# Performance work log

Hardware: AMD Instinct MI355X
Metric: run time of the kernel (lower is better)

The kernel has to match this reference:

```python
import jax, jax.numpy as jnp
from jax import lax
import numpy as np

TAU = 2.0      # LIF membrane time constant
VTH = 1.0      # spikingjelly LIFNode default v_threshold
ALPHA = 2.0    # spikingjelly surrogate.ATan default alpha

# Heaviside spike with ATan surrogate gradient (spikingjelly semantics)
@jax.custom_vjp
def spike(x):
    return (x >= 0.0).astype(x.dtype)

def _spike_fwd(x):
    return spike(x), x

def _spike_bwd(x, g):
    sg = (ALPHA / 2.0) / (1.0 + (jnp.pi / 2.0 * ALPHA * x) ** 2)
    return (g * sg,)

spike.defvjp(_spike_fwd, _spike_bwd)

def lif_step(v, x):
    # decay_input=True, v_reset=0.0, hard reset (spikingjelly LIFNode defaults)
    v = v + (x - v) / TAU
    s = spike(v - VTH)
    v = v * (1.0 - s)
    return v, s

def conv1d_same(x, k):
    # x: [N, L], k: [K]  -> depthwise-style 1D conv with SAME padding
    y = lax.conv_general_dilated(x[:, None, :], k[None, None, :], (1,), 'SAME')
    return y[:, 0, :]

def setup_inputs() -> dict:
    key = jax.random.key(0)
    ks = jax.random.split(key, 16)
    N, T, D, C, NC = 4096, 16, 700, 128, 20
    def lin(kw, kb, fout, fin):
        s = 1.0 / np.sqrt(fin)
        W = jax.random.uniform(kw, (fout, fin), jnp.float32, -s, s)
        b = jax.random.uniform(kb, (fout,), jnp.float32, -s, s)
        return W, b
    x = jax.random.normal(ks[0], (N, T, D), jnp.float32)
    W_in, b_in = lin(ks[1], ks[2], C, D)
    W_rec, b_rec = lin(ks[3], ks[4], C, C)
    W2, b2 = lin(ks[5], ks[6], C, C)
    k_t = jax.random.normal(ks[7], (3,), jnp.float32) * 0.5   # TATCA temporal conv, kernel_size_t=3
    k_c = jax.random.normal(ks[8], (3,), jnp.float32) * 0.5   # TATCA channel conv
    W_p, b_p = lin(ks[9], ks[10], C, C)
    W_out, b_out = lin(ks[11], ks[12], NC, C)
    return {"x": x, "W_in": W_in, "b_in": b_in, "W_rec": W_rec, "b_rec": b_rec,
            "W2": W2, "b2": b2, "k_t": k_t, "k_c": k_c,
            "W_p": W_p, "b_p": b_p, "W_out": W_out, "b_out": b_out}

def reference(x, W_in, b_in, W_rec, b_rec, W2, b2, k_t, k_c, W_p, b_p, W_out, b_out):
    N, T, D = x.shape
    C = W_in.shape[0]
    z = jnp.zeros((N, C), x.dtype)

    def step(carry, frame):
        v1, v2, spikes_last = carry
        inp = frame @ W_in.T + b_in + spikes_last @ W_rec.T + b_rec
        v1, s1 = lif_step(v1, inp)
        x2 = s1 @ W2.T + b2
        v2, feat = lif_step(v2, x2)
        return (v1, v2, s1), feat

    xs = jnp.transpose(x, (1, 0, 2))          # [T, N, D]
    _, features = lax.scan(step, (z, z, z), xs)  # [T, N, C]

    # TATCA_1D: temporal attention (conv over T, kernel 3) x channel attention (conv over C)
    t_att = jax.nn.sigmoid(conv1d_same(features.mean(2).T, k_t)).T   # [T, N]
    c_att = jax.nn.sigmoid(conv1d_same(features.mean(0), k_c))       # [N, C]
    attended = features * t_att[:, :, None] * c_att[None, :, :]

    def step2(v3, feat):
        h = feat @ W_p.T + b_p
        v3, s = lif_step(v3, h)
        return v3, s @ W_out.T + b_out

    _, outs = lax.scan(step2, z, attended)    # [T, N, num_classes]
    return outs.mean(0), features, attended
```

## Files before the change

kernel.cpp:

```cpp
#include <hip/hip_runtime.h>
#include <hip/hip_bf16.h>
#include <stdint.h>


typedef __attribute__((ext_vector_type(8))) _Float16 half8;
typedef __attribute__((ext_vector_type(4))) float f32x4;
typedef unsigned long long u64;

#define MFMA16F(a, b, c) __builtin_amdgcn_mfma_f32_16x16x32_f16(a, b, c, 0, 0, 0)

__device__ inline void gload16(const void* g, void* l) {
  __builtin_amdgcn_global_load_lds(
      (const __attribute__((address_space(1))) uint32_t*)g,
      (__attribute__((address_space(3))) uint32_t*)l, 16, 0, 0);
}

__device__ inline void splitf16(float4 q0, float4 q1, half8& hh, half8& ll) {
  float f[8] = {q0.x, q0.y, q0.z, q0.w, q1.x, q1.y, q1.z, q1.w};
  _Float16 H[8], L[8];
#pragma unroll
  for (int j = 0; j < 8; ++j) {
    _Float16 h1 = (_Float16)(f[j] * 16.0f);
    float r = fmaf((float)h1, -0.0625f, f[j]);
    L[j] = (_Float16)(r * 32768.0f);
    H[j] = h1;
  }
  __builtin_memcpy(&hh, H, 16);
  __builtin_memcpy(&ll, L, 16);
}

__global__ void k_prep(const float* __restrict__ Wr, const float* __restrict__ W2,
                       const float* __restrict__ Wp, const float* __restrict__ Win,
                       float* __restrict__ WrT, float* __restrict__ W2T,
                       float* __restrict__ WpT, ushort* __restrict__ F2) {
  int idx = blockIdx.x * blockDim.x + threadIdx.x;
  if (idx < 3 * 16384) {
    int sel = idx >> 14;
    int r = idx & 16383;
    int j = r >> 7, c = r & 127;
    const float* src = (sel == 0) ? Wr : (sel == 1) ? W2 : Wp;
    float* dst = (sel == 0) ? WrT : (sel == 1) ? W2T : WpT;
    dst[r] = src[c * 128 + j];
  } else {
    int i2 = idx - 49152;
    if (i2 >= 128 * 704) return;
    int c = i2 / 704, d = i2 - c * 704;
    float w = (d < 700) ? Win[c * 700 + d] : 0.f;
    _Float16 b1 = (_Float16)(w * 256.0f);
    float r = fmaf((float)b1, -0.00390625f, w);
    _Float16 b2 = (_Float16)(r * 524288.0f);
    ushort u1, u2;
    __builtin_memcpy(&u1, &b1, 2);
    __builtin_memcpy(&u2, &b2, 2);
    F2[i2] = u1;
    F2[90112 + i2] = u2;
  }
}

__global__ __launch_bounds__(512, 4) void k_gemm_mfma(
    const float* __restrict__ x, const ushort* __restrict__ F2,
    const float* __restrict__ b_in, const float* __restrict__ b_rec,
    float* __restrict__ XW) {
  __shared__ __align__(16) char lds[65536];

  const int tid = threadIdx.x;
  const int w = tid >> 6;
  const int l = tid & 63;
  const int blk = blockIdx.x;
  const int wr = w >> 2;
  const int wc = w & 3;

  const int jA = (((l & 7) ^ (l >> 3)) * 4);
  const int t_blk = (blk * 128) >> 12;
  const int n0_blk = (blk * 128) & 4095;
  int arow[2];
#pragma unroll
  for (int i = 0; i < 2; ++i) {
    int m = (w * 2 + i) * 8 + (l >> 3);
    arow[i] = ((n0_blk + m) * 16 + t_blk) * 700;
  }
  const ushort* bsrc[2];
  int bdst[2];
#pragma unroll
  for (int i = 0; i < 2; ++i) {
    int idx = w * 2 + i;
    int plane = idx >> 3, cg = idx & 7;
    int col = cg * 16 + (l >> 2);
    bsrc[i] = F2 + plane * 90112 + col * 704 + (((l & 3) ^ ((l >> 3) & 3)) * 8);
    bdst[i] = 16384 + plane * 8192 + cg * 1024;
  }
  const int adst = (w * 2) * 1024;

  const int lm = l & 15, kh = l >> 4;
  const int p0 = ((2 * kh) ^ (lm & 7)) * 16;
  const int p1 = ((2 * kh + 1) ^ (lm & 7)) * 16;
  const int bswz = (kh ^ ((lm >> 1) & 3)) * 16;
  int aoff[4], boff[2];
#pragma unroll
  for (int mf = 0; mf < 4; ++mf) aoff[mf] = (wr * 64 + mf * 16 + lm) * 128;
#pragma unroll
  for (int nf = 0; nf < 2; ++nf) boff[nf] = 16384 + (wc * 32 + nf * 16 + lm) * 64 + bswz;

  f32x4 acc_h[4][2], acc_m[4][2];
#pragma unroll
  for (int i = 0; i < 4; ++i)
#pragma unroll
    for (int j = 0; j < 2; ++j) {
      acc_h[i][j] = (f32x4){0.f, 0.f, 0.f, 0.f};
      acc_m[i][j] = (f32x4){0.f, 0.f, 0.f, 0.f};
    }

  auto STAGE = [&](int buf, int kt) {
    const int k0 = kt * 32;
    char* base = lds + buf * 32768;
#pragma unroll
    for (int i = 0; i < 2; ++i) {
      int k = k0 + jA;
      int off = (k < 700) ? (arow[i] + k) : 0;
      gload16(x + off, base + adst + i * 1024);
    }
#pragma unroll
    for (int i = 0; i < 2; ++i)
      gload16(bsrc[i] + k0, base + bdst[i]);
  };

  STAGE(0, 0);
  __syncthreads();
  int buf = 0;
  for (int kt = 0; kt < 22; ++kt) {
    if (kt + 1 < 22) STAGE(buf ^ 1, kt + 1);
    const char* base = lds + buf * 32768;
    half8 b1[2], b2[2];
#pragma unroll
    for (int nf = 0; nf < 2; ++nf) {
      const char* bb = base + boff[nf];
      b1[nf] = *(const half8*)(bb);
      b2[nf] = *(const half8*)(bb + 8192);
    }
#pragma unroll
    for (int mf = 0; mf < 4; ++mf) {
      const char* ab = base + aoff[mf];
      float4 q0 = *(const float4*)(ab + p0);
      float4 q1 = *(const float4*)(ab + p1);
      half8 a1, a2;
      splitf16(q0, q1, a1, a2);
#pragma unroll
      for (int nf = 0; nf < 2; ++nf) {
        acc_h[mf][nf] = MFMA16F(a1, b1[nf], acc_h[mf][nf]);
        acc_m[mf][nf] = MFMA16F(a1, b2[nf], acc_m[mf][nf]);
        acc_m[mf][nf] = MFMA16F(a2, b1[nf], acc_m[mf][nf]);
      }
    }
    __syncthreads();
    buf ^= 1;
  }

  const int outbase = blk * 128;
#pragma unroll
  for (int nf = 0; nf < 2; ++nf) {
    int col = wc * 32 + nf * 16 + lm;
    float bias = b_in[col] + b_rec[col];
#pragma unroll
    for (int mf = 0; mf < 4; ++mf) {
      int mrow = outbase + wr * 64 + mf * 16 + kh * 4;
#pragma unroll
      for (int r = 0; r < 4; ++r)
        XW[(size_t)(mrow + r) * 128 + col] =
            acc_h[mf][nf][r] * 0.000244140625f +
            acc_m[mf][nf][r] * 1.1920928955078125e-7f + bias;
    }
  }
}

__global__ __launch_bounds__(256) void k_scan(
    const float* __restrict__ XW, const float* __restrict__ WrT,
    const float* __restrict__ W2T, const float* __restrict__ b2,
    const float* __restrict__ WpT, const float* __restrict__ b_p,
    const float* __restrict__ W_out, const float* __restrict__ b_out,
    const float* __restrict__ k_t, const float* __restrict__ k_c,
    float* __restrict__ features, float* __restrict__ attended,
    float* __restrict__ out0) {
  const int tid = threadIdx.x;
  const int r = tid >> 7;
  const int c = tid & 127;
  const int n = blockIdx.x * 2 + r;
  const int wv = c >> 6;
  const int lane = tid & 63;

  __shared__ u64 smask[2][2];
  __shared__ u64 fmask[2][16][2];
  __shared__ float m0p[2][130];
  __shared__ float ta[2][16];
  __shared__ float ca[2][128];
  __shared__ float g[2][128];

  if (tid < 4) ((u64*)smask)[tid] = 0ull;
  float v1 = 0.f, v2 = 0.f, fsum = 0.f;
  const float b2c = b2[c];
  __syncthreads();

  for (int t = 0; t < 16; ++t) {
    float inp = XW[(size_t)((t << 12) | n) * 128 + c];
    u64 p0 = smask[r][0], p1 = smask[r][1];
    while (p0) { int j = __builtin_ctzll(p0); p0 &= p0 - 1; inp += WrT[j * 128 + c]; }
    while (p1) { int j = __builtin_ctzll(p1); p1 &= p1 - 1; inp += WrT[(64 + j) * 128 + c]; }
    v1 = v1 + (inp - v1) * 0.5f;
    bool s1 = (v1 - 1.0f) >= 0.f;
    v1 = s1 ? 0.f : v1;
    __syncthreads();
    u64 bm = __ballot((int)s1);
    if (lane == 0) smask[r][wv] = bm;
    __syncthreads();
    float x2 = b2c;
    u64 q0 = smask[r][0], q1 = smask[r][1];
    while (q0) { int j = __builtin_ctzll(q0); q0 &= q0 - 1; x2 += W2T[j * 128 + c]; }
    while (q1) { int j = __builtin_ctzll(q1); q1 &= q1 - 1; x2 += W2T[(64 + j) * 128 + c]; }
    v2 = v2 + (x2 - v2) * 0.5f;
    bool f = (v2 - 1.0f) >= 0.f;
    v2 = f ? 0.f : v2;
    float ff = f ? 1.f : 0.f;
    features[(size_t)((t << 12) | n) * 128 + c] = ff;
    fsum += ff;
    u64 fb = __ballot((int)f);
    if (lane == 0) fmask[r][t][wv] = fb;
  }

  m0p[r][c + 1] = fsum * (1.f / 16.f);
  if (c == 0) { m0p[r][0] = 0.f; m0p[r][129] = 0.f; }
  __syncthreads();

  if (c < 16) {
    float acc = 0.f;
#pragma unroll
    for (int j = 0; j < 3; ++j) {
      int tt = c - 1 + j;
      if (tt >= 0 && tt < 16) {
        float m = (float)(__popcll(fmask[r][tt][0]) + __popcll(fmask[r][tt][1])) * (1.f / 128.f);
        acc += k_t[j] * m;
      }
    }
    ta[r][c] = 1.f / (1.f + expf(-acc));
  }
  {
    float acc = k_c[0] * m0p[r][c] + k_c[1] * m0p[r][c + 1] + k_c[2] * m0p[r][c + 2];
    ca[r][c] = 1.f / (1.f + expf(-acc));
  }
  __syncthreads();

  float v3 = 0.f, ssum = 0.f;
  const float bpc = b_p[c];
  const float cac = ca[r][c];
  for (int t = 0; t < 16; ++t) {
    u64 m0 = fmask[r][t][0], m1 = fmask[r][t][1];
    float tat = ta[r][t];
    bool bit = ((wv ? m1 : m0) >> (c & 63)) & 1;
    float att = bit ? tat * cac : 0.f;
    attended[(size_t)((t << 12) | n) * 128 + c] = att;
    float h = bpc;
    while (m0) { int j = __builtin_ctzll(m0); m0 &= m0 - 1; h += (tat * ca[r][j]) * WpT[j * 128 + c]; }
    while (m1) { int j = __builtin_ctzll(m1); m1 &= m1 - 1; h += (tat * ca[r][64 + j]) * WpT[(64 + j) * 128 + c]; }
    v3 = v3 + (h - v3) * 0.5f;
    bool s = (v3 - 1.0f) >= 0.f;
    v3 = s ? 0.f : v3;
    ssum += s ? 1.f : 0.f;
  }
  g[r][c] = ssum * (1.f / 16.f);
  __syncthreads();
  if (c < 20) {
    float acc = b_out[c];
    for (int j = 0; j < 128; ++j) acc += g[r][j] * W_out[c * 128 + j];
    out0[n * 20 + c] = acc;
  }
}

extern "C" void kernel_launch(void* const* d_in, const int* in_sizes, int n_in,
                              void* d_out, int out_size, void* d_ws, size_t ws_size,
                              hipStream_t stream) {
  const float* x     = (const float*)d_in[0];
  const float* W_in  = (const float*)d_in[1];
  const float* b_in  = (const float*)d_in[2];
  const float* W_rec = (const float*)d_in[3];
  const float* b_rec = (const float*)d_in[4];
  const float* W2    = (const float*)d_in[5];
  const float* b2    = (const float*)d_in[6];
  const float* k_t   = (const float*)d_in[7];
  const float* k_c   = (const float*)d_in[8];
  const float* W_p   = (const float*)d_in[9];
  const float* b_p   = (const float*)d_in[10];
  const float* W_out = (const float*)d_in[11];
  const float* b_out = (const float*)d_in[12];

  float* out      = (float*)d_out;
  float* out0     = out;
  float* features = out + 81920;
  float* attended = out + 81920 + 8388608;
  float* XW       = attended;

  float* ws  = (float*)d_ws;
  float* WrT = ws;
  float* W2T = ws + 16384;
  float* WpT = ws + 32768;
  ushort* F2 = (ushort*)(ws + 49152);

  hipLaunchKernelGGL(k_prep, dim3(544), dim3(256), 0, stream,
                     W_rec, W2, W_p, W_in, WrT, W2T, WpT, F2);
  hipLaunchKernelGGL(k_gemm_mfma, dim3(512), dim3(512), 0, stream,
                     x, F2, b_in, b_rec, XW);
  hipLaunchKernelGGL(k_scan, dim3(2048), dim3(256), 0, stream,
                     XW, WrT, W2T, b2, WpT, b_p, W_out, b_out, k_t, k_c,
                     features, attended, out0);
}
```

Baseline: 92.99 us.

## Fuse input GEMM with LIF scan via LDS-resident XW tiles

Merges the MFMA input-projection GEMM and the recurrent scan into one kernel. Each block now computes 128 rows as 8 samples × 16 timesteps, so every sample's full time series stays in the block, and the projection is staged in LDS instead of round-tripping through global memory. This removes the XW write and read and one launch. In exchange the scan runs with only 512 blocks of 4 samples per chunk in two serial chunks, which cuts parallelism for the latency-bound scan and adds block-wide barriers.

```diff
diff --git a/kernel.cpp b/kernel.cpp
--- a/kernel.cpp
+++ b/kernel.cpp
@@ -57,10 +57,15 @@
   }
 }
 
-__global__ __launch_bounds__(512, 4) void k_gemm_mfma(
+__global__ __launch_bounds__(512, 4) void k_gemm_scan(
     const float* __restrict__ x, const ushort* __restrict__ F2,
     const float* __restrict__ b_in, const float* __restrict__ b_rec,
-    float* __restrict__ XW) {
+    const float* __restrict__ WrT, const float* __restrict__ W2T,
+    const float* __restrict__ b2, const float* __restrict__ WpT,
+    const float* __restrict__ b_p, const float* __restrict__ W_out,
+    const float* __restrict__ b_out, const float* __restrict__ k_t,
+    const float* __restrict__ k_c, float* __restrict__ features,
+    float* __restrict__ attended, float* __restrict__ out0) {
   __shared__ __align__(16) char lds[65536];
 
   const int tid = threadIdx.x;
@@ -71,14 +76,10 @@
   const int wc = w & 3;
 
   const int jA = (((l & 7) ^ (l >> 3)) * 4);
-  const int t_blk = (blk * 128) >> 12;
-  const int n0_blk = (blk * 128) & 4095;
   int arow[2];
 #pragma unroll
-  for (int i = 0; i < 2; ++i) {
-    int m = (w * 2 + i) * 8 + (l >> 3);
-    arow[i] = ((n0_blk + m) * 16 + t_blk) * 700;
-  }
+  for (int i = 0; i < 2; ++i)
+    arow[i] = (blk * 128 + (w * 2 + i) * 8 + (l >> 3)) * 700;
   const ushort* bsrc[2];
   int bdst[2];
 #pragma unroll
@@ -130,12 +131,12 @@
   for (int kt = 0; kt < 22; ++kt) {
     if (kt + 1 < 22) STAGE(buf ^ 1, kt + 1);
     const char* base = lds + buf * 32768;
-    half8 b1[2], b2[2];
+    half8 b1[2], b2f[2];
 #pragma unroll
     for (int nf = 0; nf < 2; ++nf) {
       const char* bb = base + boff[nf];
       b1[nf] = *(const half8*)(bb);
-      b2[nf] = *(const half8*)(bb + 8192);
+      b2f[nf] = *(const half8*)(bb + 8192);
     }
 #pragma unroll
     for (int mf = 0; mf < 4; ++mf) {
@@ -147,7 +148,7 @@
 #pragma unroll
       for (int nf = 0; nf < 2; ++nf) {
         acc_h[mf][nf] = MFMA16F(a1, b1[nf], acc_h[mf][nf]);
-        acc_m[mf][nf] = MFMA16F(a1, b2[nf], acc_m[mf][nf]);
+        acc_m[mf][nf] = MFMA16F(a1, b2f[nf], acc_m[mf][nf]);
         acc_m[mf][nf] = MFMA16F(a2, b1[nf], acc_m[mf][nf]);
       }
     }
@@ -155,121 +156,124 @@
     buf ^= 1;
   }
 
-  const int outbase = blk * 128;
+  float bias[2];
 #pragma unroll
   for (int nf = 0; nf < 2; ++nf) {
     int col = wc * 32 + nf * 16 + lm;
-    float bias = b_in[col] + b_rec[col];
-#pragma unroll
-    for (int mf = 0; mf < 4; ++mf) {
-      int mrow = outbase + wr * 64 + mf * 16 + kh * 4;
-#pragma unroll
-      for (int r = 0; r < 4; ++r)
-        XW[(size_t)(mrow + r) * 128 + col] =
-            acc_h[mf][nf][r] * 0.000244140625f +
-            acc_m[mf][nf][r] * 1.1920928955078125e-7f + bias;
-    }
-  }
-}
-
-__global__ __launch_bounds__(256) void k_scan(
-    const float* __restrict__ XW, const float* __restrict__ WrT,
-    const float* __restrict__ W2T, const float* __restrict__ b2,
-    const float* __restrict__ WpT, const float* __restrict__ b_p,
-    const float* __restrict__ W_out, const float* __restrict__ b_out,
-    const float* __restrict__ k_t, const float* __restrict__ k_c,
-    float* __restrict__ features, float* __restrict__ attended,
-    float* __restrict__ out0) {
-  const int tid = threadIdx.x;
-  const int r = tid >> 7;
+    bias[nf] = b_in[col] + b_rec[col];
+  }
+
+  float* XWs = (float*)lds;
+  u64* smaskp = (u64*)(lds + 33792);
+  u64* fmaskp = (u64*)(lds + 33856);
+  float* tap = (float*)(lds + 34880);
+  float* m0p = (float*)(lds + 35136);
+  float* cap = (float*)(lds + 37216);
+  float* gp = (float*)(lds + 39264);
+
+  const int s = tid >> 7;
   const int c = tid & 127;
-  const int n = blockIdx.x * 2 + r;
-  const int wv = c >> 6;
+  const int wv = (tid >> 6) & 1;
   const int lane = tid & 63;
-
-  __shared__ u64 smask[2][2];
-  __shared__ u64 fmask[2][16][2];
-  __shared__ float m0p[2][130];
-  __shared__ float ta[2][16];
-  __shared__ float ca[2][128];
-  __shared__ float g[2][128];
-
-  if (tid < 4) ((u64*)smask)[tid] = 0ull;
-  float v1 = 0.f, v2 = 0.f, fsum = 0.f;
   const float b2c = b2[c];
-  __syncthreads();
-
-  for (int t = 0; t < 16; ++t) {
-    float inp = XW[(size_t)((t << 12) | n) * 128 + c];
-    u64 p0 = smask[r][0], p1 = smask[r][1];
-    while (p0) { int j = __builtin_ctzll(p0); p0 &= p0 - 1; inp += WrT[j * 128 + c]; }
-    while (p1) { int j = __builtin_ctzll(p1); p1 &= p1 - 1; inp += WrT[(64 + j) * 128 + c]; }
-    v1 = v1 + (inp - v1) * 0.5f;
-    bool s1 = (v1 - 1.0f) >= 0.f;
-    v1 = s1 ? 0.f : v1;
-    __syncthreads();
-    u64 bm = __ballot((int)s1);
-    if (lane == 0) smask[r][wv] = bm;
-    __syncthreads();
-    float x2 = b2c;
-    u64 q0 = smask[r][0], q1 = smask[r][1];
-    while (q0) { int j = __builtin_ctzll(q0); q0 &= q0 - 1; x2 += W2T[j * 128 + c]; }
-    while (q1) { int j = __builtin_ctzll(q1); q1 &= q1 - 1; x2 += W2T[(64 + j) * 128 + c]; }
-    v2 = v2 + (x2 - v2) * 0.5f;
-    bool f = (v2 - 1.0f) >= 0.f;
-    v2 = f ? 0.f : v2;
-    float ff = f ? 1.f : 0.f;
-    features[(size_t)((t << 12) | n) * 128 + c] = ff;
-    fsum += ff;
-    u64 fb = __ballot((int)f);
-    if (lane == 0) fmask[r][t][wv] = fb;
-  }
-
-  m0p[r][c + 1] = fsum * (1.f / 16.f);
-  if (c == 0) { m0p[r][0] = 0.f; m0p[r][129] = 0.f; }
-  __syncthreads();
-
-  if (c < 16) {
-    float acc = 0.f;
-#pragma unroll
-    for (int j = 0; j < 3; ++j) {
-      int tt = c - 1 + j;
-      if (tt >= 0 && tt < 16) {
-        float m = (float)(__popcll(fmask[r][tt][0]) + __popcll(fmask[r][tt][1])) * (1.f / 128.f);
-        acc += k_t[j] * m;
+  const float bpc = b_p[c];
+
+  for (int chunk = 0; chunk < 2; ++chunk) {
+    __syncthreads();
+    if (tid < 8) smaskp[tid] = 0ull;
+    if (wr == chunk) {
+#pragma unroll
+      for (int nf = 0; nf < 2; ++nf) {
+        int col = wc * 32 + nf * 16 + lm;
+#pragma unroll
+        for (int mf = 0; mf < 4; ++mf) {
+          int rowl = mf * 16 + kh * 4;
+#pragma unroll
+          for (int r = 0; r < 4; ++r)
+            XWs[(rowl + r) * 132 + col] =
+                acc_h[mf][nf][r] * 0.000244140625f +
+                acc_m[mf][nf][r] * 1.1920928955078125e-7f + bias[nf];
+        }
       }
     }
-    ta[r][c] = 1.f / (1.f + expf(-acc));
-  }
-  {
-    float acc = k_c[0] * m0p[r][c] + k_c[1] * m0p[r][c + 1] + k_c[2] * m0p[r][c + 2];
-    ca[r][c] = 1.f / (1.f + expf(-acc));
-  }
-  __syncthreads();
-
-  float v3 = 0.f, ssum = 0.f;
-  const float bpc = b_p[c];
-  const float cac = ca[r][c];
-  for (int t = 0; t < 16; ++t) {
-    u64 m0 = fmask[r][t][0], m1 = fmask[r][t][1];
-    float tat = ta[r][t];
-    bool bit = ((wv ? m1 : m0) >> (c & 63)) & 1;
-    float att = bit ? tat * cac : 0.f;
-    attended[(size_t)((t << 12) | n) * 128 + c] = att;
-    float h = bpc;
-    while (m0) { int j = __builtin_ctzll(m0); m0 &= m0 - 1; h += (tat * ca[r][j]) * WpT[j * 128 + c]; }
-    while (m1) { int j = __builtin_ctzll(m1); m1 &= m1 - 1; h += (tat * ca[r][64 + j]) * WpT[(64 + j) * 128 + c]; }
-    v3 = v3 + (h - v3) * 0.5f;
-    bool s = (v3 - 1.0f) >= 0.f;
-    v3 = s ? 0.f : v3;
-    ssum += s ? 1.f : 0.f;
-  }
-  g[r][c] = ssum * (1.f / 16.f);
-  __syncthreads();
-  if (c < 20) {
-    float acc = b_out[c];
-    for (int j = 0; j < 128; ++j) acc += g[r][j] * W_out[c * 128 + j];
-    out0[n * 20 + c] = acc;
+    __syncthreads();
+
+    const int n_glob = blk * 8 + chunk * 4 + s;
+    float v1 = 0.f, v2 = 0.f, fsum = 0.f;
+
+    for (int t = 0; t < 16; ++t) {
+      float inp = XWs[(s * 16 + t) * 132 + c];
+      u64 pm0 = smaskp[s * 2 + 0], pm1 = smaskp[s * 2 + 1];
+      while (pm0) { int j = __builtin_ctzll(pm0); pm0 &= pm0 - 1; inp += WrT[j * 128 + c]; }
+      while (pm1) { int j = __builtin_ctzll(pm1); pm1 &= pm1 - 1; inp += WrT[(64 + j) * 128 + c]; }
+      v1 = v1 + (inp - v1) * 0.5f;
+      bool s1 = (v1 - 1.0f) >= 0.f;
+      v1 = s1 ? 0.f : v1;
+      __syncthreads();
+      u64 bm = __ballot((int)s1);
+      if (lane == 0) smaskp[s * 2 + wv] = bm;
+      __syncthreads();
+      float x2 = b2c;
+      u64 q0 = smaskp[s * 2 + 0], q1 = smaskp[s * 2 + 1];
+      while (q0) { int j = __builtin_ctzll(q0); q0 &= q0 - 1; x2 += W2T[j * 128 + c]; }
+      while (q1) { int j = __builtin_ctzll(q1); q1 &= q1 - 1; x2 += W2T[(64 + j) * 128 + c]; }
+      v2 = v2 + (x2 - v2) * 0.5f;
+      bool f = (v2 - 1.0f) >= 0.f;
+      v2 = f ? 0.f : v2;
+      float ff = f ? 1.f : 0.f;
+      features[(size_t)((t << 12) | n_glob) * 128 + c] = ff;
+      fsum += ff;
+      u64 fb = __ballot((int)f);
+      if (lane == 0) fmaskp[(s * 16 + t) * 2 + wv] = fb;
+    }
+
+    m0p[s * 130 + c + 1] = fsum * (1.f / 16.f);
+    if (c == 0) { m0p[s * 130 + 0] = 0.f; m0p[s * 130 + 129] = 0.f; }
+    __syncthreads();
+
+    if (c < 16) {
+      float acc = 0.f;
+#pragma unroll
+      for (int j = 0; j < 3; ++j) {
+        int tt = c - 1 + j;
+        if (tt >= 0 && tt < 16) {
+          float m = (float)(__popcll(fmaskp[(s * 16 + tt) * 2 + 0]) +
+                            __popcll(fmaskp[(s * 16 + tt) * 2 + 1])) * (1.f / 128.f);
+          acc += k_t[j] * m;
+        }
+      }
+      tap[s * 16 + c] = 1.f / (1.f + expf(-acc));
+    }
+    {
+      float acc = k_c[0] * m0p[s * 130 + c] + k_c[1] * m0p[s * 130 + c + 1] +
+                  k_c[2] * m0p[s * 130 + c + 2];
+      cap[s * 128 + c] = 1.f / (1.f + expf(-acc));
+    }
+    __syncthreads();
+
+    float v3 = 0.f, ssum = 0.f;
+    const float cac = cap[s * 128 + c];
+    for (int t = 0; t < 16; ++t) {
+      u64 m0 = fmaskp[(s * 16 + t) * 2 + 0], m1 = fmaskp[(s * 16 + t) * 2 + 1];
+      float tat = tap[s * 16 + t];
+      bool bit = ((wv ? m1 : m0) >> (c & 63)) & 1;
+      float att = bit ? tat * cac : 0.f;
+      attended[(size_t)((t << 12) | n_glob) * 128 + c] = att;
+      float h = bpc;
+      while (m0) { int j = __builtin_ctzll(m0); m0 &= m0 - 1; h += (tat * cap[s * 128 + j]) * WpT[j * 128 + c]; }
+      while (m1) { int j = __builtin_ctzll(m1); m1 &= m1 - 1; h += (tat * cap[s * 128 + 64 + j]) * WpT[(64 + j) * 128 + c]; }
+      v3 = v3 + (h - v3) * 0.5f;
+      bool sp = (v3 - 1.0f) >= 0.f;
+      v3 = sp ? 0.f : v3;
+      ssum += sp ? 1.f : 0.f;
+    }
+    gp[s * 128 + c] = ssum * (1.f / 16.f);
+    __syncthreads();
+    if (c < 20) {
+      float acc = b_out[c];
+      for (int j = 0; j < 128; ++j) acc += gp[s * 128 + j] * W_out[c * 128 + j];
+      out0[n_glob * 20 + c] = acc;
+    }
   }
 }
 
@@ -294,7 +298,6 @@
   float* out0     = out;
   float* features = out + 81920;
   float* attended = out + 81920 + 8388608;
-  float* XW       = attended;
 
   float* ws  = (float*)d_ws;
   float* WrT = ws;
@@ -304,9 +307,7 @@
 
   hipLaunchKernelGGL(k_prep, dim3(544), dim3(256), 0, stream,
                      W_rec, W2, W_p, W_in, WrT, W2T, WpT, F2);
-  hipLaunchKernelGGL(k_gemm_mfma, dim3(512), dim3(512), 0, stream,
-                     x, F2, b_in, b_rec, XW);
-  hipLaunchKernelGGL(k_scan, dim3(2048), dim3(256), 0, stream,
-                     XW, WrT, W2T, b2, WpT, b_p, W_out, b_out, k_t, k_c,
-                     features, attended, out0);
-}
+  hipLaunchKernelGGL(k_gemm_scan, dim3(512), dim3(512), 0, stream,
+                     x, F2, b_in, b_rec, WrT, W2T, b2, WpT, b_p, W_out, b_out,
+                     k_t, k_c, features, attended, out0);
+}
```

Result: no change. 94.47 us (+1.6%).
